# Performance work log

Measured on AMD Instinct MI355X. Metric: run time of the kernel, lower is better.

## Reference

```python
import jax, jax.numpy as jnp
import numpy as np

IN, H = 40, 64

def setup_inputs() -> dict:
    key = jax.random.key(0)
    ks = jax.random.split(key, 10)
    s_ih = 1.0 / np.sqrt(H)
    return {
        "x": jax.random.normal(ks[0], (1024, 500, IN), dtype=jnp.float32),
        "W_ih": jax.random.uniform(ks[1], (4 * H, IN), minval=-s_ih, maxval=s_ih, dtype=jnp.float32),
        "W_hh": jax.random.uniform(ks[2], (4 * H, H), minval=-s_ih, maxval=s_ih, dtype=jnp.float32),
        "b_ih": jax.random.uniform(ks[3], (4 * H,), minval=-s_ih, maxval=s_ih, dtype=jnp.float32),
        "b_hh": jax.random.uniform(ks[4], (4 * H,), minval=-s_ih, maxval=s_ih, dtype=jnp.float32),
        "fc1_w": jax.random.uniform(ks[5], (H, H), minval=-s_ih, maxval=s_ih, dtype=jnp.float32),
        "fc1_b": jax.random.uniform(ks[6], (H,), minval=-s_ih, maxval=s_ih, dtype=jnp.float32),
        "fc2_w": jax.random.uniform(ks[7], (2, H), minval=-s_ih, maxval=s_ih, dtype=jnp.float32),
        "fc2_b": jax.random.uniform(ks[8], (2,), minval=-s_ih, maxval=s_ih, dtype=jnp.float32),
    }

def _lstm_last_hidden(x, W_ih, W_hh, b_ih, b_hh):
    B = x.shape[0]
    # Precompute input projections for all timesteps in one big GEMM: [B,T,4H]
    x_proj = jnp.einsum('bti,gi->btg', x, W_ih) + (b_ih + b_hh)
    x_proj_t = jnp.swapaxes(x_proj, 0, 1)  # [T,B,4H] for scan over time

    def step(carry, xp):
        h, c = carry
        z = xp + h @ W_hh.T  # [B,4H], PyTorch gate order: i,f,g,o
        i = jax.nn.sigmoid(z[:, 0 * H:1 * H])
        f = jax.nn.sigmoid(z[:, 1 * H:2 * H])
        g = jnp.tanh(z[:, 2 * H:3 * H])
        o = jax.nn.sigmoid(z[:, 3 * H:4 * H])
        c = f * c + i * g
        h = o * jnp.tanh(c)
        return (h, c), None

    h0 = jnp.zeros((B, H), dtype=x.dtype)
    (h_last, _), _ = jax.lax.scan(step, (h0, h0), x_proj_t)
    return h_last  # [B,H]

def reference(x, W_ih, W_hh, b_ih, b_hh, fc1_w, fc1_b, fc2_w, fc2_b):
    h = _lstm_last_hidden(x, W_ih, W_hh, b_ih, b_hh)
    h = jax.nn.relu(h @ fc1_w.T + fc1_b)
    return h @ fc2_w.T + fc2_b  # [B,2]
```

## Files before the change

### kernel.cpp

```cpp
#include <hip/hip_runtime.h>

#define IN_DIM 40
#define HID 64
#define TSTEPS 500
#define CHAINS 16
#define KDIM 128

typedef _Float16 half2v __attribute__((ext_vector_type(2)));
typedef _Float16 half8  __attribute__((ext_vector_type(8)));
typedef float    f32x4  __attribute__((ext_vector_type(4)));

__device__ __forceinline__ float sigmoid_fast(float x) {
    return __builtin_amdgcn_rcpf(1.0f + __expf(-x));
}

__device__ __forceinline__ float tanh_fast(float x) {
    float ax = fabsf(x);
    float e = __expf(-2.0f * ax);
    float r = (1.0f - e) * __builtin_amdgcn_rcpf(1.0f + e);
    return copysignf(r, x);
}

__device__ __forceinline__ void block_sync_lds() {
    asm volatile("s_waitcnt lgkmcnt(0)" ::: "memory");
    __builtin_amdgcn_s_barrier();
    __builtin_amdgcn_sched_barrier(0);
}

__global__ __launch_bounds__(256, 1)
void lstm_mfma(const float* __restrict__ x,
               const float* __restrict__ W_ih,
               const float* __restrict__ W_hh,
               const float* __restrict__ b_ih,
               const float* __restrict__ b_hh,
               const float* __restrict__ fc1_w,
               const float* __restrict__ fc1_b,
               const float* __restrict__ fc2_w,
               const float* __restrict__ fc2_b,
               float* __restrict__ out)
{
    const int tid = threadIdx.x;
    const int w   = tid >> 6;
    const int l   = tid & 63;
    const int lr  = l & 15;
    const int lg  = l >> 4;
    const int blk = blockIdx.x;

    __shared__ __align__(16) unsigned short slab[2][CHAINS][KDIM];
    __shared__ float h32[CHAINS][HID];
    __shared__ float rl [CHAINS][HID];

    {
        uint4* p = reinterpret_cast<uint4*>(slab);
        p[tid]       = uint4{0, 0, 0, 0};
        p[tid + 256] = uint4{0, 0, 0, 0};
    }

    half8 wfrag[4][4];
    float biasr[4][4];
    #pragma unroll
    for (int j = 0; j < 4; ++j) {
        const int jt   = 4 * w + j;
        const int unit = 4 * jt + (lr >> 2);
        const int gate = lr & 3;
        const int row  = gate * HID + unit;
        #pragma unroll
        for (int kt = 0; kt < 4; ++kt) {
            const int k0 = kt * 32 + lg * 8;
            float v[8];
            if (k0 < 64) {
                const float4* p = reinterpret_cast<const float4*>(W_hh + (size_t)row * HID + k0);
                float4 q0 = p[0], q1 = p[1];
                v[0]=q0.x; v[1]=q0.y; v[2]=q0.z; v[3]=q0.w;
                v[4]=q1.x; v[5]=q1.y; v[6]=q1.z; v[7]=q1.w;
            } else if (k0 < 104) {
                const float4* p = reinterpret_cast<const float4*>(W_ih + (size_t)row * IN_DIM + (k0 - 64));
                float4 q0 = p[0], q1 = p[1];
                v[0]=q0.x; v[1]=q0.y; v[2]=q0.z; v[3]=q0.w;
                v[4]=q1.x; v[5]=q1.y; v[6]=q1.z; v[7]=q1.w;
            } else {
                #pragma unroll
                for (int e = 0; e < 8; ++e) v[e] = 0.0f;
            }
            half8 hv;
            #pragma unroll
            for (int e = 0; e < 8; ++e) hv[e] = (_Float16)v[e];
            wfrag[j][kt] = hv;
        }
        const int ud = 4 * jt + lg;
        #pragma unroll
        for (int r = 0; r < 4; ++r)
            biasr[j][r] = b_ih[r * HID + ud] + b_hh[r * HID + ud];
    }

    const int  xc   = tid / 10;
    const int  xseg = tid - xc * 10;
    const bool xact = (tid < 160);
    const float* xgbase = x + ((size_t)(blk * CHAINS + xc) * TSTEPS) * IN_DIM + xseg * 4;
    const int  xoff = xc * 256 + ((128 + 8 * xseg) ^ ((xc & 7) << 4));

    auto xstore = [&](int par, const float4& v) {
        half2v lo = { (_Float16)v.x, (_Float16)v.y };
        half2v hi = { (_Float16)v.z, (_Float16)v.w };
        uint2 o = { __builtin_bit_cast(uint, lo), __builtin_bit_cast(uint, hi) };
        *reinterpret_cast<uint2*>(reinterpret_cast<char*>(slab) + par * 4096 + xoff) = o;
    };

    float4 fA = {0,0,0,0}, fB = {0,0,0,0};
    if (xact) {
        float4 x0 = *reinterpret_cast<const float4*>(xgbase);
        xstore(0, x0);
        fA = *reinterpret_cast<const float4*>(xgbase + IN_DIM);
    }
    __syncthreads();

    float cs[4] = {0.f, 0.f, 0.f, 0.f};
    float hreg[4];

    auto step = [&](int t, int par, const float4& cur, float4& nxt) {
        const bool lastt = (t == TSTEPS - 1);
        if (xact) {
            const int tp = (t + 2 < TSTEPS) ? t + 2 : TSTEPS - 1;
            nxt = *reinterpret_cast<const float4*>(xgbase + (size_t)tp * IN_DIM);
        }
        half8 bf[4];
        #pragma unroll
        for (int kt = 0; kt < 4; ++kt) {
            const int addr = par * 4096 + lr * 256 + (((kt * 64) + lg * 16) ^ ((lr & 7) << 4));
            uint4 q = *reinterpret_cast<const uint4*>(reinterpret_cast<const char*>(slab) + addr);
            bf[kt] = __builtin_bit_cast(half8, q);
        }
        #pragma unroll
        for (int j = 0; j < 4; ++j) {
            f32x4 acc = { biasr[j][0], biasr[j][1], biasr[j][2], biasr[j][3] };
            #pragma unroll
            for (int kt = 0; kt < 4; ++kt)
                acc = __builtin_amdgcn_mfma_f32_16x16x32_f16(wfrag[j][kt], bf[kt], acc, 0, 0, 0);
            float iv = sigmoid_fast(acc[0]);
            float fv = sigmoid_fast(acc[1]);
            float gv = tanh_fast(acc[2]);
            float ov = sigmoid_fast(acc[3]);
            cs[j] = fmaf(fv, cs[j], iv * gv);
            hreg[j] = ov * tanh_fast(cs[j]);
        }
        if (lastt) {
            #pragma unroll
            for (int j = 0; j < 4; ++j)
                h32[lr][4 * (4 * w + j) + lg] = hreg[j];
        } else {
            #pragma unroll
            for (int j = 0; j < 4; ++j) {
                const int u = 4 * (4 * w + j) + lg;
                const int haddr = (par ^ 1) * 4096 + lr * 256 + ((u * 2) ^ ((lr & 7) << 4));
                _Float16 hf = (_Float16)hreg[j];
                *reinterpret_cast<unsigned short*>(reinterpret_cast<char*>(slab) + haddr) =
                    __builtin_bit_cast(unsigned short, hf);
            }
            if (xact) xstore(par ^ 1, cur);
        }
        block_sync_lds();
    };

    #pragma unroll 1
    for (int t = 0; t < TSTEPS; t += 2) {
        step(t,     0, fA, fB);
        step(t + 1, 1, fB, fA);
    }

    {
        float4 wrow[16];
        const float4* fwp = reinterpret_cast<const float4*>(fc1_w + (size_t)l * HID);
        #pragma unroll
        for (int q = 0; q < 16; ++q) wrow[q] = fwp[q];
        const float b1 = fc1_b[l];
        #pragma unroll
        for (int cc = 0; cc < 4; ++cc) {
            const int chain = 4 * w + cc;
            float acc = b1;
            #pragma unroll
            for (int q = 0; q < 16; ++q) {
                float4 hv = reinterpret_cast<const float4*>(&h32[chain][0])[q];
                acc = fmaf(wrow[q].x, hv.x, acc);
                acc = fmaf(wrow[q].y, hv.y, acc);
                acc = fmaf(wrow[q].z, hv.z, acc);
                acc = fmaf(wrow[q].w, hv.w, acc);
            }
            rl[chain][l] = fmaxf(acc, 0.0f);
        }
    }
    __syncthreads();
    if (tid < 32) {
        const int c = tid >> 1;
        const int o = tid & 1;
        float acc = fc2_b[o];
        for (int k = 0; k < HID; ++k)
            acc = fmaf(fc2_w[o * HID + k], rl[c][k], acc);
        out[(size_t)(blk * CHAINS + c) * 2 + o] = acc;
    }
}

extern "C" void kernel_launch(void* const* d_in, const int* in_sizes, int n_in,
                              void* d_out, int out_size, void* d_ws, size_t ws_size,
                              hipStream_t stream) {
    const float* x     = (const float*)d_in[0];
    const float* W_ih  = (const float*)d_in[1];
    const float* W_hh  = (const float*)d_in[2];
    const float* b_ih  = (const float*)d_in[3];
    const float* b_hh  = (const float*)d_in[4];
    const float* fc1_w = (const float*)d_in[5];
    const float* fc1_b = (const float*)d_in[6];
    const float* fc2_w = (const float*)d_in[7];
    const float* fc2_b = (const float*)d_in[8];
    float* out = (float*)d_out;

    const int B = in_sizes[0] / (TSTEPS * IN_DIM);
    lstm_mfma<<<B / CHAINS, 256, 0, stream>>>(x, W_ih, W_hh, b_ih, b_hh,
                                              fc1_w, fc1_b, fc2_w, fc2_b, out);
}
```

Measured before the change: 282.6 us.

## Feed x directly into MFMA registers instead of staging through LDS

Each lane now loads its own x fragment from global memory, converts it to fp16 in registers, and passes it straight to the two input-projection MFMAs. This drops the shared-memory staging of x, the xor swizzle and the LDS writes. The LDS slab shrinks to hidden state only, using a padded row stride of 144 bytes in place of the swizzle. It also relaxes the barrier's scheduling fence to a memory clobber, and orders the x MFMAs first so they can run before the hidden-state LDS reads arrive. The costs are more redundant global loads per lane and a prefetch distance of one step, down from two.

```diff
diff --git a/kernel.cpp b/kernel.cpp
--- a/kernel.cpp
+++ b/kernel.cpp
@@ -4,11 +4,10 @@
 #define HID 64
 #define TSTEPS 500
 #define CHAINS 16
-#define KDIM 128
-
-typedef _Float16 half2v __attribute__((ext_vector_type(2)));
-typedef _Float16 half8  __attribute__((ext_vector_type(8)));
-typedef float    f32x4  __attribute__((ext_vector_type(4)));
+#define ROWB 144
+
+typedef _Float16 half8 __attribute__((ext_vector_type(8)));
+typedef float    f32x4 __attribute__((ext_vector_type(4)));
 
 __device__ __forceinline__ float sigmoid_fast(float x) {
     return __builtin_amdgcn_rcpf(1.0f + __expf(-x));
@@ -24,7 +23,7 @@
 __device__ __forceinline__ void block_sync_lds() {
     asm volatile("s_waitcnt lgkmcnt(0)" ::: "memory");
     __builtin_amdgcn_s_barrier();
-    __builtin_amdgcn_sched_barrier(0);
+    asm volatile("" ::: "memory");
 }
 
 __global__ __launch_bounds__(256, 1)
@@ -46,18 +45,19 @@
     const int lg  = l >> 4;
     const int blk = blockIdx.x;
 
-    __shared__ __align__(16) unsigned short slab[2][CHAINS][KDIM];
+    __shared__ __align__(16) unsigned char slab[2][CHAINS * ROWB];
     __shared__ float h32[CHAINS][HID];
     __shared__ float rl [CHAINS][HID];
 
     {
-        uint4* p = reinterpret_cast<uint4*>(slab);
-        p[tid]       = uint4{0, 0, 0, 0};
-        p[tid + 256] = uint4{0, 0, 0, 0};
+        uint4 z{0, 0, 0, 0};
+        uint4* zp = reinterpret_cast<uint4*>(slab);
+        zp[tid] = z;
+        if (tid < 32) zp[256 + tid] = z;
     }
 
     half8 wfrag[4][4];
-    float biasr[4][4];
+    f32x4 biasr[4];
     #pragma unroll
     for (int j = 0; j < 4; ++j) {
         const int jt   = 4 * w + j;
@@ -88,59 +88,57 @@
             wfrag[j][kt] = hv;
         }
         const int ud = 4 * jt + lg;
-        #pragma unroll
-        for (int r = 0; r < 4; ++r)
-            biasr[j][r] = b_ih[r * HID + ud] + b_hh[r * HID + ud];
-    }
-
-    const int  xc   = tid / 10;
-    const int  xseg = tid - xc * 10;
-    const bool xact = (tid < 160);
-    const float* xgbase = x + ((size_t)(blk * CHAINS + xc) * TSTEPS) * IN_DIM + xseg * 4;
-    const int  xoff = xc * 256 + ((128 + 8 * xseg) ^ ((xc & 7) << 4));
-
-    auto xstore = [&](int par, const float4& v) {
-        half2v lo = { (_Float16)v.x, (_Float16)v.y };
-        half2v hi = { (_Float16)v.z, (_Float16)v.w };
-        uint2 o = { __builtin_bit_cast(uint, lo), __builtin_bit_cast(uint, hi) };
-        *reinterpret_cast<uint2*>(reinterpret_cast<char*>(slab) + par * 4096 + xoff) = o;
-    };
-
-    float4 fA = {0,0,0,0}, fB = {0,0,0,0};
-    if (xact) {
-        float4 x0 = *reinterpret_cast<const float4*>(xgbase);
-        xstore(0, x0);
-        fA = *reinterpret_cast<const float4*>(xgbase + IN_DIM);
-    }
+        biasr[j] = f32x4{ b_ih[0 * HID + ud] + b_hh[0 * HID + ud],
+                          b_ih[1 * HID + ud] + b_hh[1 * HID + ud],
+                          b_ih[2 * HID + ud] + b_hh[2 * HID + ud],
+                          b_ih[3 * HID + ud] + b_hh[3 * HID + ud] };
+    }
+
+    const float* xrow = x + ((size_t)(blk * CHAINS + lr) * TSTEPS) * IN_DIM;
+    const float* xg2  = xrow + lg * 8;
+    const float* xg3  = xrow + 32;
+
+    float4 a0, a1, a2, a3, b0, b1, b2, b3;
+    a0 = *reinterpret_cast<const float4*>(xg2);
+    a1 = *reinterpret_cast<const float4*>(xg2 + 4);
+    a2 = *reinterpret_cast<const float4*>(xg3);
+    a3 = *reinterpret_cast<const float4*>(xg3 + 4);
+
     __syncthreads();
 
     float cs[4] = {0.f, 0.f, 0.f, 0.f};
     float hreg[4];
 
-    auto step = [&](int t, int par, const float4& cur, float4& nxt) {
+    auto step = [&](int t, int par,
+                    const float4& c0, const float4& c1, const float4& c2, const float4& c3,
+                    float4& n0, float4& n1, float4& n2, float4& n3) {
         const bool lastt = (t == TSTEPS - 1);
-        if (xact) {
-            const int tp = (t + 2 < TSTEPS) ? t + 2 : TSTEPS - 1;
-            nxt = *reinterpret_cast<const float4*>(xgbase + (size_t)tp * IN_DIM);
-        }
-        half8 bf[4];
-        #pragma unroll
-        for (int kt = 0; kt < 4; ++kt) {
-            const int addr = par * 4096 + lr * 256 + (((kt * 64) + lg * 16) ^ ((lr & 7) << 4));
-            uint4 q = *reinterpret_cast<const uint4*>(reinterpret_cast<const char*>(slab) + addr);
-            bf[kt] = __builtin_bit_cast(half8, q);
-        }
+        const unsigned char* sp = &slab[par][0] + lr * ROWB + lg * 16;
+        uint4 q0 = *reinterpret_cast<const uint4*>(sp);
+        uint4 q1 = *reinterpret_cast<const uint4*>(sp + 64);
+        const size_t toff = (size_t)(lastt ? t : t + 1) * IN_DIM;
+        n0 = *reinterpret_cast<const float4*>(xg2 + toff);
+        n1 = *reinterpret_cast<const float4*>(xg2 + toff + 4);
+        n2 = *reinterpret_cast<const float4*>(xg3 + toff);
+        n3 = *reinterpret_cast<const float4*>(xg3 + toff + 4);
+        half8 xf2 = { (_Float16)c0.x, (_Float16)c0.y, (_Float16)c0.z, (_Float16)c0.w,
+                      (_Float16)c1.x, (_Float16)c1.y, (_Float16)c1.z, (_Float16)c1.w };
+        half8 xf3 = { (_Float16)c2.x, (_Float16)c2.y, (_Float16)c2.z, (_Float16)c2.w,
+                      (_Float16)c3.x, (_Float16)c3.y, (_Float16)c3.z, (_Float16)c3.w };
+        half8 bf0 = __builtin_bit_cast(half8, q0);
+        half8 bf1 = __builtin_bit_cast(half8, q1);
         #pragma unroll
         for (int j = 0; j < 4; ++j) {
-            f32x4 acc = { biasr[j][0], biasr[j][1], biasr[j][2], biasr[j][3] };
-            #pragma unroll
-            for (int kt = 0; kt < 4; ++kt)
-                acc = __builtin_amdgcn_mfma_f32_16x16x32_f16(wfrag[j][kt], bf[kt], acc, 0, 0, 0);
+            f32x4 acc = biasr[j];
+            acc = __builtin_amdgcn_mfma_f32_16x16x32_f16(wfrag[j][2], xf2, acc, 0, 0, 0);
+            acc = __builtin_amdgcn_mfma_f32_16x16x32_f16(wfrag[j][3], xf3, acc, 0, 0, 0);
+            acc = __builtin_amdgcn_mfma_f32_16x16x32_f16(wfrag[j][0], bf0, acc, 0, 0, 0);
+            acc = __builtin_amdgcn_mfma_f32_16x16x32_f16(wfrag[j][1], bf1, acc, 0, 0, 0);
             float iv = sigmoid_fast(acc[0]);
             float fv = sigmoid_fast(acc[1]);
             float gv = tanh_fast(acc[2]);
             float ov = sigmoid_fast(acc[3]);
-            cs[j] = fmaf(fv, cs[j], iv * gv);
+            cs[j]   = fmaf(fv, cs[j], iv * gv);
             hreg[j] = ov * tanh_fast(cs[j]);
         }
         if (lastt) {
@@ -148,23 +146,22 @@
             for (int j = 0; j < 4; ++j)
                 h32[lr][4 * (4 * w + j) + lg] = hreg[j];
         } else {
+            unsigned char* dp = &slab[par ^ 1][0] + lr * ROWB;
             #pragma unroll
             for (int j = 0; j < 4; ++j) {
                 const int u = 4 * (4 * w + j) + lg;
-                const int haddr = (par ^ 1) * 4096 + lr * 256 + ((u * 2) ^ ((lr & 7) << 4));
                 _Float16 hf = (_Float16)hreg[j];
-                *reinterpret_cast<unsigned short*>(reinterpret_cast<char*>(slab) + haddr) =
+                *reinterpret_cast<unsigned short*>(dp + u * 2) =
                     __builtin_bit_cast(unsigned short, hf);
             }
-            if (xact) xstore(par ^ 1, cur);
         }
         block_sync_lds();
     };
 
     #pragma unroll 1
     for (int t = 0; t < TSTEPS; t += 2) {
-        step(t,     0, fA, fB);
-        step(t + 1, 1, fB, fA);
+        step(t,     0, a0, a1, a2, a3, b0, b1, b2, b3);
+        step(t + 1, 1, b0, b1, b2, b3, a0, a1, a2, a3);
     }
 
     {
```

After: 413.3 us. 1.46x slower.
